# Kernel tuning notes

Measured on AMD Instinct MI355X. Metric: run time of the kernel, lower is better.

Reference implementation:

```python
import jax, jax.numpy as jnp
import numpy as np

N_NODES = 20000
N_EDGES = 160000
B = 200      # num graphs (nodes per graph = 100)
T = 8        # num_tau
A = 10       # action_size
H = 4        # heads
D = 128      # out_channels
R = 4        # num_relations
NCOS = 64


def rgat(x, edge_index, edge_type, W, q, k, b):
    # W: [R, in, H*D]; q, k: [H*D, H]; b: [D]
    xw = jnp.einsum('ni,rio->nro', x, W)              # [N, R, H*D]
    src, dst = edge_index[0], edge_index[1]
    xj = xw[src, edge_type]                            # [E, H*D] gather by edge + relation
    xi = xw[dst, edge_type]                            # [E, H*D]
    alpha = jax.nn.leaky_relu(xi @ q + xj @ k, 0.2)    # [E, H]
    amax = jax.ops.segment_max(alpha, dst, num_segments=N_NODES)
    ex = jnp.exp(alpha - amax[dst])                    # segment softmax over dst
    denom = jax.ops.segment_sum(ex, dst, num_segments=N_NODES)
    a = ex / denom[dst]                                # [E, H]
    msg = (a[:, :, None] * xj.reshape(-1, H, D)).reshape(-1, H * D)
    agg = jax.ops.segment_sum(msg, dst, num_segments=N_NODES).reshape(-1, H, D)
    return agg.mean(axis=1) + b                        # concat=False -> mean over heads


def noisy_linear(z, w, bias, sw, sb, ew, eb):
    # torch convention: w [out, in]
    return z @ (w + sw * ew).T + (bias + sb * eb)


def setup_inputs():
    key = jax.random.key(0)
    ks = jax.random.split(key, 48)
    def rn(i, shape, scale=0.05):
        return jax.random.normal(ks[i], shape, dtype=jnp.float32) * scale
    SIG = 0.017
    inp = {
        'x': jax.random.normal(ks[0], (N_NODES, 2), dtype=jnp.float32),
        'edge_index': jax.random.randint(ks[1], (2, N_EDGES), 0, N_NODES, dtype=jnp.int32),
        'edge_type': jax.random.randint(ks[2], (N_EDGES,), 0, R, dtype=jnp.int32),
        'taus': jax.random.uniform(ks[3], (B, T, 1), dtype=jnp.float32),
        'W1': rn(4, (R, 2, H * D), 0.3), 'q1': rn(5, (H * D, H), 0.05), 'k1': rn(6, (H * D, H), 0.05), 'b1': rn(7, (D,)),
        'W2': rn(8, (R, D, H * D), 0.06), 'q2': rn(9, (H * D, H), 0.05), 'k2': rn(10, (H * D, H), 0.05), 'b2': rn(11, (D,)),
        'cos_w': rn(12, (D, NCOS), 0.1), 'cos_b': rn(13, (D,)),
        'ff1_w': rn(14, (D, D), 0.1), 'ff1_b': rn(15, (D,)),
        'ff1_sw': jnp.full((D, D), SIG, jnp.float32), 'ff1_sb': jnp.full((D,), SIG, jnp.float32),
        'ff1_ew': rn(16, (D, D), 1.0), 'ff1_eb': rn(17, (D,), 1.0),
        'ff2_w': rn(18, (D, D), 0.1), 'ff2_b': rn(19, (D,)),
        'ff2_sw': jnp.full((D, D), SIG, jnp.float32), 'ff2_sb': jnp.full((D,), SIG, jnp.float32),
        'ff2_ew': rn(20, (D, D), 1.0), 'ff2_eb': rn(21, (D,), 1.0),
        'adv_w': rn(22, (A, D), 0.1), 'adv_b': rn(23, (A,)),
        'adv_sw': jnp.full((A, D), SIG, jnp.float32), 'adv_sb': jnp.full((A,), SIG, jnp.float32),
        'adv_ew': rn(24, (A, D), 1.0), 'adv_eb': rn(25, (A,), 1.0),
        'val_w': rn(26, (1, D), 0.1), 'val_b': rn(27, (1,)),
        'val_sw': jnp.full((1, D), SIG, jnp.float32), 'val_sb': jnp.full((1,), SIG, jnp.float32),
        'val_ew': rn(28, (1, D), 1.0), 'val_eb': rn(29, (1,), 1.0),
    }
    return inp


def reference(x, edge_index, edge_type, taus,
              W1, q1, k1, b1, W2, q2, k2, b2, cos_w, cos_b,
              ff1_w, ff1_b, ff1_sw, ff1_sb, ff1_ew, ff1_eb,
              ff2_w, ff2_b, ff2_sw, ff2_sb, ff2_ew, ff2_eb,
              adv_w, adv_b, adv_sw, adv_sb, adv_ew, adv_eb,
              val_w, val_b, val_sw, val_sb, val_ew, val_eb):
    h = jax.nn.selu(rgat(x, edge_index, edge_type, W1, q1, k1, b1))
    h = jax.nn.selu(rgat(h, edge_index, edge_type, W2, q2, k2, b2))
    g = h.reshape(B, N_NODES // B, D).sum(axis=1)      # global_add_pool (block batch_idx)
    pis = jnp.pi * jnp.arange(1, NCOS + 1, dtype=jnp.float32)  # [NCOS]
    cos = jnp.cos(taus * pis)                           # [B, T, NCOS]
    cos_x = jax.nn.relu(cos @ cos_w.T + cos_b)          # [B, T, D]
    z = (g[:, None, :] * cos_x).reshape(B * T, D)
    z = jax.nn.selu(noisy_linear(z, ff1_w, ff1_b, ff1_sw, ff1_sb, ff1_ew, ff1_eb))
    z = jax.nn.selu(noisy_linear(z, ff2_w, ff2_b, ff2_sw, ff2_sb, ff2_ew, ff2_eb))
    adv = noisy_linear(z, adv_w, adv_b, adv_sw, adv_sb, adv_ew, adv_eb)   # [B*T, A]
    val = noisy_linear(z, val_w, val_b, val_sw, val_sb, val_ew, val_eb)   # [B*T, 1]
    out = val + adv - adv.mean(axis=1, keepdims=True)
    return out.reshape(B, T, A), taus
```

## Files before the change

### kernel.cpp

```cpp
#include <hip/hip_runtime.h>
#include <hip/hip_bf16.h>

constexpr long NN = 20000;
constexpr long NE = 160000;
constexpr long BB = 200;
constexpr long TT = 8;
constexpr long GN = 100;

constexpr long O_FLAG = 0;
constexpr long O_X    = 16;                 constexpr long N_X   = 40000;
constexpr long O_TAU  = O_X + N_X;          constexpr long N_TAU = 1600;
constexpr long O_W1   = O_TAU + N_TAU;      constexpr long N_W1  = 4096;
constexpr long O_Q1   = O_W1 + N_W1;        constexpr long N_Q   = 2048;
constexpr long O_K1   = O_Q1 + N_Q;
constexpr long O_B1   = O_K1 + N_Q;         constexpr long N_B   = 128;
constexpr long O_W2   = O_B1 + N_B;         constexpr long N_W2  = 262144;
constexpr long O_Q2   = O_W2 + N_W2;
constexpr long O_K2   = O_Q2 + N_Q;
constexpr long O_B2   = O_K2 + N_Q;
constexpr long O_CW   = O_B2 + N_B;         constexpr long N_CW  = 8192;
constexpr long O_CB   = O_CW + N_CW;
constexpr long O_F1W  = O_CB + N_B;         constexpr long N_FW  = 16384;
constexpr long O_F1B  = O_F1W + N_FW;
constexpr long O_F1SW = O_F1B + N_B;
constexpr long O_F1SB = O_F1SW + N_FW;
constexpr long O_F1EW = O_F1SB + N_B;
constexpr long O_F1EB = O_F1EW + N_FW;
constexpr long O_F2W  = O_F1EB + N_B;
constexpr long O_F2B  = O_F2W + N_FW;
constexpr long O_F2SW = O_F2B + N_B;
constexpr long O_F2SB = O_F2SW + N_FW;
constexpr long O_F2EW = O_F2SB + N_B;
constexpr long O_F2EB = O_F2EW + N_FW;
constexpr long O_AW   = O_F2EB + N_B;       constexpr long N_AW  = 1280;
constexpr long O_AB   = O_AW + N_AW;        constexpr long N_AB  = 16;
constexpr long O_ASW  = O_AB + N_AB;
constexpr long O_ASB  = O_ASW + N_AW;
constexpr long O_AEW  = O_ASB + N_AB;
constexpr long O_AEB  = O_AEW + N_AW;
constexpr long O_VW   = O_AEB + N_AB;       constexpr long N_VW  = 128;
constexpr long O_VB   = O_VW + N_VW;        constexpr long N_VB  = 16;
constexpr long O_VSW  = O_VB + N_VB;
constexpr long O_VSB  = O_VSW + N_VW;
constexpr long O_VEW  = O_VSB + N_VB;
constexpr long O_VEB  = O_VEW + N_VW;
constexpr long O_WQ1  = O_VEB + N_VB;
constexpr long O_WK1  = O_WQ1 + 32;
constexpr long O_WQ2  = O_WK1 + 32;
constexpr long O_WK2  = O_WQ2 + 2048;
constexpr long O_CF1W = O_WK2 + 2048;
constexpr long O_CF1B = O_CF1W + N_FW;
constexpr long O_CF2W = O_CF1B + N_B;
constexpr long O_CF2B = O_CF2W + N_FW;
constexpr long O_CAW  = O_CF2B + N_B;
constexpr long O_CAB  = O_CAW + N_AW;
constexpr long O_CVW  = O_CAB + N_AB;
constexpr long O_CVB  = O_CVW + N_VW;
constexpr long O_AL1  = O_CVB + N_VB;
constexpr long O_AL2  = O_AL1 + NE*4;
constexpr long O_H1   = O_AL2 + NE*4;
constexpr long O_H2   = O_H1 + NN*128;
constexpr long O_G    = O_H2 + NN*128;
constexpr long O_Z0   = O_G + BB*128;
constexpr long O_Z1   = O_Z0 + BB*TT*128;
constexpr long O_Z2   = O_Z1 + BB*TT*128;
constexpr long O_AGG1 = O_Z2 + BB*TT*128;
constexpr long O_DEG  = O_AGG1;
constexpr long O_CUR  = O_DEG + NN;
constexpr long O_ROWP = O_CUR + NN;
constexpr long O_PERM = O_ROWP + NN + 8;
constexpr long O_AGG2 = O_AGG1 + NN*128;
constexpr long O_DEN1 = O_AGG2 + NN*128;
constexpr long O_DEN2 = O_DEN1 + NN*4;
constexpr long O_AMAX1= O_DEN2 + NN*4;
constexpr long O_AMAX2= O_AMAX1 + NN*4;
constexpr long O_XW2  = O_AMAX2 + NN*4;
constexpr long O_END_TABLE = O_XW2 + (NN*4*512)/2;
constexpr long MPAD   = 20096;
constexpr long O_H1B  = O_END_TABLE;
constexpr long O_W2BT = O_H1B + (MPAD*128)/2;
constexpr long O_END2 = O_W2BT + (2048L*128)/2;
constexpr long O_AQ   = O_END2;
constexpr long O_AK   = O_AQ + NN*16;
constexpr long O_END3 = O_AK + NN*16;

constexpr int EMAX = 128;

#define DEVFN __device__ __forceinline__

typedef __attribute__((ext_vector_type(8))) short bf16x8;
typedef __attribute__((ext_vector_type(4))) float f32x4;
typedef __attribute__((ext_vector_type(4))) unsigned short u16x4;

DEVFN float selu_f(float x){ return 1.0507009873554805f * (x > 0.f ? x : 1.6732632423543772f * expm1f(x)); }
DEVFN float lrelu_f(float x){ return x >= 0.f ? x : 0.2f * x; }
DEVFN float bf2f(unsigned short u){ return __uint_as_float(((unsigned)u) << 16); }

__global__ void k_detect(const unsigned short* taus_u16, int* flag){
    if (threadIdx.x == 0){
        int bf = 1;
        for (int i = 0; i < 128; i++){
            if (taus_u16[i] > 0x3F80u){ bf = 0; break; }
        }
        *flag = bf;
    }
}

struct ConvArgs { const void* src[38]; long off[38]; int n[38]; };

__global__ void k_convert(ConvArgs a, float* ws){
    int arr = blockIdx.y;
    long off = a.off[arr];
    if (off < 0) return;
    const void* s = a.src[arr];
    int n = a.n[arr];
    int bf = ((const int*)ws)[0];
    for (int i = blockIdx.x*blockDim.x + threadIdx.x; i < n; i += gridDim.x*blockDim.x){
        float v;
        if (bf){ unsigned short u = ((const unsigned short*)s)[i]; v = bf2f(u); }
        else   { v = ((const float*)s)[i]; }
        ws[off + i] = v;
    }
}

__global__ void k_hist(const int* ei, float* ws){
    long e = (long)blockIdx.x*blockDim.x + threadIdx.x;
    if (e >= NE) return;
    atomicAdd((int*)(ws + O_DEG) + ei[NE + e], 1);
}

__global__ void k_scan(float* ws){
    const int* deg = (const int*)(ws + O_DEG);
    int* rowp = (int*)(ws + O_ROWP);
    __shared__ int part[256];
    int tid = threadIdx.x;
    int base = tid * 79;
    int n = 0; if (base < NN) n = min(79, (int)NN - base);
    int s = 0;
    for (int i = 0; i < n; i++) s += deg[base + i];
    part[tid] = s;
    __syncthreads();
    if (tid == 0){
        int acc = 0;
        for (int i = 0; i < 256; i++){ int t = part[i]; part[i] = acc; acc += t; }
    }
    __syncthreads();
    int acc = part[tid];
    for (int i = 0; i < n; i++){ rowp[base + i] = acc; acc += deg[base + i]; }
    if (tid == 0) rowp[NN] = (int)NE;
}

__global__ void k_scatter(const int* ei, float* ws){
    long e = (long)blockIdx.x*blockDim.x + threadIdx.x;
    if (e >= NE) return;
    int dst = ei[NE + e];
    int pos = atomicAdd((int*)(ws + O_CUR) + dst, 1);
    ((int*)(ws + O_PERM))[((const int*)(ws + O_ROWP))[dst] + pos] = (int)e;
}

__global__ void k_prep(float* ws){
    int phase = blockIdx.y;
    int idx = blockIdx.x*blockDim.x + threadIdx.x;
    if (phase == 0){
        if (idx >= 4160) return;
        long wsrc, qsrc, dst; int ri, h;
        if (idx < 64){
            int t = idx & 31; h = t & 3; ri = t >> 2;
            wsrc = O_W1 + (long)ri*512;
            qsrc = (idx < 32) ? O_Q1 : O_K1;
            dst  = ((idx < 32) ? O_WQ1 : O_WK1) + t;
        } else {
            int t = (idx - 64) & 2047; h = t & 3; ri = t >> 2;
            wsrc = O_W2 + (long)ri*512;
            qsrc = (idx < 2112) ? O_Q2 : O_K2;
            dst  = ((idx < 2112) ? O_WQ2 : O_WK2) + t;
        }
        const float* W = ws + wsrc;
        const float* Q = ws + qsrc;
        float s = 0.f;
        for (int o = 0; o < 512; o++) s += W[o] * Q[o*4 + h];
        ws[dst] = s;
    } else if (phase == 1){
        const long tw[8] = {O_F1W,O_F2W,O_AW,O_VW, O_F1B,O_F2B,O_AB,O_VB};
        const long ts[8] = {O_F1SW,O_F2SW,O_ASW,O_VSW, O_F1SB,O_F2SB,O_ASB,O_VSB};
        const long te[8] = {O_F1EW,O_F2EW,O_AEW,O_VEW, O_F1EB,O_F2EB,O_AEB,O_VEB};
        const long td[8] = {O_CF1W,O_CF2W,O_CAW,O_CVW, O_CF1B,O_CF2B,O_CAB,O_CVB};
        const int  tn[8] = {16384,16384,1280,128, 128,128,10,1};
        const int  tb[8] = {0,16384,32768,34048, 34176,34304,34432,34442};
        int total = 34443;
        for (int i = idx; i < total; i += gridDim.x*blockDim.x){
            int t = 0;
            #pragma unroll
            for (int q = 1; q < 8; q++) if (i >= tb[q]) t = q;
            int j = i - tb[t];
            if (j < tn[t]) ws[td[t] + j] = ws[tw[t] + j] + ws[ts[t] + j]*ws[te[t] + j];
        }
    } else if (phase == 2){
        if (idx >= 262144) return;
        int np = idx & 2047, k = idx >> 11;
        int r = np >> 9, q = np & 511, d = q >> 2, h = q & 3;
        float v = ws[O_W2 + (long)r*65536 + (long)k*512 + h*128 + d];
        ((__hip_bfloat16*)(ws + O_W2BT))[(long)np*128 + k] = __float2bfloat16(v);
    } else {
        if (idx < 6144) ws[O_H1B + (20000L*128)/2 + idx] = 0.f;
    }
}

__global__ void k_node1(const int* ei, const int* et, float* ws){
    __shared__ float wqk[64];
    __shared__ float alc[EMAX][4];
    __shared__ float xsc[EMAX][2];
    __shared__ int   rtc[EMAX];
    __shared__ float sacc[4][4][2];
    __shared__ float den[4], amax[4];
    __shared__ float mred[2][4];
    int n = blockIdx.x, tid = threadIdx.x;
    const int* rowp = (const int*)(ws + O_ROWP);
    const int* perm = (const int*)(ws + O_PERM);
    int e0 = rowp[n], deg = rowp[n+1] - e0;
    if (tid < 64) wqk[tid] = ws[O_WQ1 + tid];
    if (tid < 32) ((float*)sacc)[tid] = 0.f;
    if (tid < 4) den[tid] = 0.f;
    float xd0 = ws[O_X + (long)n*2], xd1 = ws[O_X + (long)n*2 + 1];
    __syncthreads();
    float mx[4] = {-3.0e38f,-3.0e38f,-3.0e38f,-3.0e38f};
    for (int j0 = 0; j0 < deg; j0 += 128){
        int j = j0 + tid;
        if (j < deg){
            int e = perm[e0 + j];
            int src = ei[e], rt = et[e];
            float xs0 = ws[O_X + (long)src*2], xs1 = ws[O_X + (long)src*2 + 1];
            const float* Wq = wqk + rt*8;
            const float* Wk = wqk + 32 + rt*8;
            #pragma unroll
            for (int h = 0; h < 4; h++){
                float a = lrelu_f(xd0*Wq[h] + xd1*Wq[4+h] + xs0*Wk[h] + xs1*Wk[4+h]);
                if (j < EMAX) alc[j][h] = a;
                mx[h] = fmaxf(mx[h], a);
            }
            if (j < EMAX){ xsc[j][0] = xs0; xsc[j][1] = xs1; rtc[j] = rt; }
        }
    }
    #pragma unroll
    for (int off = 32; off > 0; off >>= 1)
        #pragma unroll
        for (int h = 0; h < 4; h++) mx[h] = fmaxf(mx[h], __shfl_xor(mx[h], off));
    if ((tid & 63) == 0)
        #pragma unroll
        for (int h = 0; h < 4; h++) mred[tid >> 6][h] = mx[h];
    __syncthreads();
    if (tid < 4) amax[tid] = fmaxf(mred[0][tid], mred[1][tid]);
    __syncthreads();
    for (int j0 = 0; j0 < deg; j0 += 128){
        int j = j0 + tid;
        if (j < deg){
            float al[4], xs0, xs1; int rt;
            if (j < EMAX){
                #pragma unroll
                for (int h = 0; h < 4; h++) al[h] = alc[j][h];
                xs0 = xsc[j][0]; xs1 = xsc[j][1]; rt = rtc[j];
            } else {
                int e = perm[e0 + j];
                int src = ei[e]; rt = et[e];
                xs0 = ws[O_X + (long)src*2]; xs1 = ws[O_X + (long)src*2 + 1];
                const float* Wq = wqk + rt*8;
                const float* Wk = wqk + 32 + rt*8;
                #pragma unroll
                for (int h = 0; h < 4; h++)
                    al[h] = lrelu_f(xd0*Wq[h] + xd1*Wq[4+h] + xs0*Wk[h] + xs1*Wk[4+h]);
            }
            #pragma unroll
            for (int h = 0; h < 4; h++){
                float ex = expf(al[h] - amax[h]);
                atomicAdd(&den[h], ex);
                atomicAdd(&sacc[rt][h][0], ex*xs0);
                atomicAdd(&sacc[rt][h][1], ex*xs1);
            }
        }
    }
    __syncthreads();
    int d = tid;
    float rden[4];
    #pragma unroll
    for (int h = 0; h < 4; h++) rden[h] = den[h] > 0.f ? 0.25f/den[h] : 0.f;
    float v = 0.f;
    #pragma unroll
    for (int r = 0; r < 4; r++)
        #pragma unroll
        for (int h = 0; h < 4; h++){
            float w0 = ws[O_W1 + r*1024 +        h*128 + d];
            float w1 = ws[O_W1 + r*1024 + 512  + h*128 + d];
            v += rden[h]*(w0*sacc[r][h][0] + w1*sacc[r][h][1]);
        }
    float out = selu_f(v + ws[O_B1 + d]);
    ws[O_H1 + (long)n*128 + d] = out;
    ((__hip_bfloat16*)(ws + O_H1B))[(long)n*128 + d] = __float2bfloat16(out);
}

__global__ void k_aqk(float* ws){
    __shared__ float wq[128*16];
    __shared__ float wk[128*16];
    __shared__ float hl[16][129];
    int tid = threadIdx.x;
    long nb = (long)blockIdx.x * 16;
    #pragma unroll
    for (int c = 0; c < 8; c++){
        int idx = tid + c*256;
        int i = idx >> 4, o = idx & 15;
        int r = o >> 2, h = o & 3;
        wq[i*16 + o] = ws[O_WQ2 + r*512 + i*4 + h];
        wk[i*16 + o] = ws[O_WK2 + r*512 + i*4 + h];
        hl[idx >> 7][idx & 127] = ws[O_H1 + nb*128 + idx];
    }
    __syncthreads();
    int j = tid >> 4, o = tid & 15;
    float aq = 0.f, ak = 0.f;
    #pragma unroll 4
    for (int i = 0; i < 128; i++){
        float hv = hl[j][i];
        aq += hv * wq[i*16 + o];
        ak += hv * wk[i*16 + o];
    }
    ws[O_AQ + (nb + j)*16 + o] = aq;
    ws[O_AK + (nb + j)*16 + o] = ak;
}

__global__ void k_xw2_mfma(float* ws){
    __shared__ __align__(16) unsigned short Ash[128*128];
    __shared__ __align__(16) unsigned short Bsh[128*128];
    const unsigned short* h1b  = (const unsigned short*)(ws + O_H1B);
    const unsigned short* w2bt = (const unsigned short*)(ws + O_W2BT);
    long bm = (long)blockIdx.x * 128;
    long bn = (long)blockIdx.y * 128;
    int tid = threadIdx.x;
    char* Ac = (char*)Ash; char* Bc = (char*)Bsh;
    #pragma unroll
    for (int i = 0; i < 8; i++){
        int c = tid + i*256;
        int row = c >> 4, kb = (c & 15) * 16;
        int off = row*256 + (kb ^ ((row & 7) << 4));
        *(bf16x8*)(Ac + off) = *(const bf16x8*)&h1b [(bm + row)*128 + (c & 15)*8];
        *(bf16x8*)(Bc + off) = *(const bf16x8*)&w2bt[(bn + row)*128 + (c & 15)*8];
    }
    __syncthreads();
    int w = tid >> 6, lane = tid & 63;
    int wm = (w >> 1) * 64, wn = (w & 1) * 64;
    int r16 = lane & 15, kq = lane >> 4;
    f32x4 acc[4][4] = {};
    #pragma unroll
    for (int ks = 0; ks < 4; ks++){
        int kbyte = ks*64 + kq*16;
        bf16x8 a[4], b[4];
        #pragma unroll
        for (int m = 0; m < 4; m++){
            int row = wm + m*16 + r16;
            a[m] = *(const bf16x8*)(Ac + row*256 + (kbyte ^ ((row & 7) << 4)));
        }
        #pragma unroll
        for (int n = 0; n < 4; n++){
            int row = wn + n*16 + r16;
            b[n] = *(const bf16x8*)(Bc + row*256 + (kbyte ^ ((row & 7) << 4)));
        }
        #pragma unroll
        for (int m = 0; m < 4; m++)
            #pragma unroll
            for (int n = 0; n < 4; n++)
                acc[m][n] = __builtin_amdgcn_mfma_f32_16x16x32_bf16(a[m], b[n], acc[m][n], 0, 0, 0);
    }
    __hip_bfloat16* xb = (__hip_bfloat16*)(ws + O_XW2);
    #pragma unroll
    for (int m = 0; m < 4; m++){
        long gr0 = bm + wm + m*16 + kq*4;
        #pragma unroll
        for (int j = 0; j < 4; j++){
            long gr = gr0 + j;
            if (gr < NN){
                #pragma unroll
                for (int n = 0; n < 4; n++){
                    long gc = bn + wn + n*16 + r16;
                    xb[gr*2048 + gc] = __float2bfloat16(acc[m][n][j]);
                }
            }
        }
    }
}

__global__ void k_node2(const int* ei, const int* et, float* ws){
    __shared__ float aq[16];
    __shared__ float exc[EMAX][4];
    __shared__ int   esrt[EMAX];
    __shared__ float den[4], amax[4];
    __shared__ float mred[2][4];
    int n = blockIdx.x, tid = threadIdx.x;
    const int* rowp = (const int*)(ws + O_ROWP);
    const int* perm = (const int*)(ws + O_PERM);
    int e0 = rowp[n], deg = rowp[n+1] - e0;
    if (tid < 16) aq[tid] = ws[O_AQ + (long)n*16 + tid];
    if (tid < 4) den[tid] = 0.f;
    __syncthreads();
    float mx[4] = {-3.0e38f,-3.0e38f,-3.0e38f,-3.0e38f};
    for (int j0 = 0; j0 < deg; j0 += 128){
        int j = j0 + tid;
        if (j < deg){
            int e = perm[e0 + j];
            int src = ei[e], rt = et[e];
            float4 k4 = *(const float4*)&ws[O_AK + (long)src*16 + rt*4];
            float al0 = lrelu_f(aq[rt*4+0] + k4.x);
            float al1 = lrelu_f(aq[rt*4+1] + k4.y);
            float al2 = lrelu_f(aq[rt*4+2] + k4.z);
            float al3 = lrelu_f(aq[rt*4+3] + k4.w);
            if (j < EMAX){
                exc[j][0]=al0; exc[j][1]=al1; exc[j][2]=al2; exc[j][3]=al3;
                esrt[j] = src*4 + rt;
            }
            mx[0]=fmaxf(mx[0],al0); mx[1]=fmaxf(mx[1],al1);
            mx[2]=fmaxf(mx[2],al2); mx[3]=fmaxf(mx[3],al3);
        }
    }
    #pragma unroll
    for (int off = 32; off > 0; off >>= 1)
        #pragma unroll
        for (int h = 0; h < 4; h++) mx[h] = fmaxf(mx[h], __shfl_xor(mx[h], off));
    if ((tid & 63) == 0)
        #pragma unroll
        for (int h = 0; h < 4; h++) mred[tid >> 6][h] = mx[h];
    __syncthreads();
    if (tid < 4) amax[tid] = fmaxf(mred[0][tid], mred[1][tid]);
    __syncthreads();
    for (int j0 = 0; j0 < deg; j0 += 128){
        int j = j0 + tid;
        if (j < deg && j < EMAX){
            #pragma unroll
            for (int h = 0; h < 4; h++){
                float ex = expf(exc[j][h] - amax[h]);
                exc[j][h] = ex;
                atomicAdd(&den[h], ex);
            }
        } else if (j < deg){
            int e = perm[e0 + j];
            int src = ei[e], rt = et[e];
            float4 k4 = *(const float4*)&ws[O_AK + (long)src*16 + rt*4];
            float al[4] = {lrelu_f(aq[rt*4+0]+k4.x), lrelu_f(aq[rt*4+1]+k4.y),
                           lrelu_f(aq[rt*4+2]+k4.z), lrelu_f(aq[rt*4+3]+k4.w)};
            #pragma unroll
            for (int h = 0; h < 4; h++) atomicAdd(&den[h], expf(al[h]-amax[h]));
        }
    }
    __syncthreads();
    int d = tid;
    const unsigned short* xw2 = (const unsigned short*)(ws + O_XW2);
    float acc[4] = {0.f,0.f,0.f,0.f};
    for (int j = 0; j < deg; j++){
        float ex[4]; long sr;
        if (j < EMAX){
            ex[0]=exc[j][0]; ex[1]=exc[j][1]; ex[2]=exc[j][2]; ex[3]=exc[j][3];
            sr = esrt[j];
        } else {
            int e = perm[e0 + j];
            int src = ei[e], rt = et[e];
            float4 k4 = *(const float4*)&ws[O_AK + (long)src*16 + rt*4];
            ex[0]=expf(lrelu_f(aq[rt*4+0]+k4.x)-amax[0]);
            ex[1]=expf(lrelu_f(aq[rt*4+1]+k4.y)-amax[1]);
            ex[2]=expf(lrelu_f(aq[rt*4+2]+k4.z)-amax[2]);
            ex[3]=expf(lrelu_f(aq[rt*4+3]+k4.w)-amax[3]);
            sr = (long)src*4 + rt;
        }
        u16x4 v = *(const u16x4*)(xw2 + sr*512 + (d << 2));
        acc[0] += ex[0]*bf2f(v[0]);
        acc[1] += ex[1]*bf2f(v[1]);
        acc[2] += ex[2]*bf2f(v[2]);
        acc[3] += ex[3]*bf2f(v[3]);
    }
    float v = 0.f;
    #pragma unroll
    for (int h = 0; h < 4; h++){
        float rden = den[h] > 0.f ? 0.25f/den[h] : 0.f;
        v += acc[h]*rden;
    }
    ws[O_H2 + (long)n*128 + d] = selu_f(v + ws[O_B2 + d]);
}

__global__ void k_pool(float* ws){
    int b = blockIdx.x, d = threadIdx.x;
    float s = 0.f;
    for (int j = 0; j < GN; j++) s += ws[O_H2 + ((long)b*GN + j)*128 + d];
    ws[O_G + (long)b*128 + d] = s;
}

__global__ void k_tail(float* ws, void* d_out, const void* taus_raw){
    __shared__ float cs[64];
    __shared__ float row0[128], row1[128], row2[128];
    __shared__ float advs[12];
    int bt = blockIdx.x, t = threadIdx.x;
    int b = bt >> 3;
    if (t < 64){
        float tau = ws[O_TAU + bt];
        cs[t] = cosf(tau * (3.14159265358979323846f * (float)(t + 1)));
    }
    __syncthreads();
    {
        const float* cw = ws + O_CW + (long)t*64;
        float s = ws[O_CB + t];
        for (int c = 0; c < 64; c++) s += cs[c]*cw[c];
        s = fmaxf(s, 0.f);
        row0[t] = ws[O_G + (long)b*128 + t] * s;
    }
    __syncthreads();
    {
        const float* W = ws + O_CF1W + (long)t*128;
        float s = ws[O_CF1B + t];
        for (int i = 0; i < 128; i++) s += row0[i]*W[i];
        row1[t] = selu_f(s);
    }
    __syncthreads();
    {
        const float* W = ws + O_CF2W + (long)t*128;
        float s = ws[O_CF2B + t];
        for (int i = 0; i < 128; i++) s += row1[i]*W[i];
        row2[t] = selu_f(s);
    }
    __syncthreads();
    if (t < 11){
        const float* W = (t < 10) ? (ws + O_CAW + (long)t*128) : (ws + O_CVW);
        float s = (t < 10) ? ws[O_CAB + t] : ws[O_CVB];
        for (int i = 0; i < 128; i++) s += row2[i]*W[i];
        advs[t] = s;
    }
    __syncthreads();
    if (t == 0){
        float m = 0.f;
        #pragma unroll
        for (int a = 0; a < 10; a++) m += advs[a];
        m *= 0.1f;
        float val = advs[10];
        int bf = ((const int*)ws)[0];
        if (bf){
            __hip_bfloat16* out = (__hip_bfloat16*)d_out;
            for (int a = 0; a < 10; a++) out[(long)bt*10 + a] = __float2bfloat16(val + advs[a] - m);
            ((unsigned short*)d_out)[16000 + bt] = ((const unsigned short*)taus_raw)[bt];
        } else {
            float* out = (float*)d_out;
            for (int a = 0; a < 10; a++) out[(long)bt*10 + a] = val + advs[a] - m;
            out[16000 + bt] = ((const float*)taus_raw)[bt];
        }
    }
}

extern "C" void kernel_launch(void* const* d_in, const int* in_sizes, int n_in,
                              void* d_out, int out_size, void* d_ws, size_t ws_size,
                              hipStream_t stream){
    (void)in_sizes; (void)n_in; (void)out_size; (void)ws_size;
    float* ws = (float*)d_ws;
    const int* ei = (const int*)d_in[1];
    const int* et = (const int*)d_in[2];

    hipMemsetAsync(ws + O_DEG, 0, (size_t)(2*NN)*4, stream);

    k_detect<<<1, 64, 0, stream>>>((const unsigned short*)d_in[3], (int*)d_ws);

    k_hist<<<625, 256, 0, stream>>>(ei, ws);
    k_scan<<<1, 256, 0, stream>>>(ws);
    k_scatter<<<625, 256, 0, stream>>>(ei, ws);

    ConvArgs ca;
    static const long conv_o[38] = {
        O_X, -1, -1, O_TAU, O_W1, O_Q1, O_K1, O_B1, O_W2, O_Q2, O_K2, O_B2, O_CW, O_CB,
        O_F1W, O_F1B, O_F1SW, O_F1SB, O_F1EW, O_F1EB,
        O_F2W, O_F2B, O_F2SW, O_F2SB, O_F2EW, O_F2EB,
        O_AW, O_AB, O_ASW, O_ASB, O_AEW, O_AEB,
        O_VW, O_VB, O_VSW, O_VSB, O_VEW, O_VEB };
    static const int conv_n[38] = {
        40000, 0, 0, 1600, 4096, 2048, 2048, 128, 262144, 2048, 2048, 128, 8192, 128,
        16384, 128, 16384, 128, 16384, 128,
        16384, 128, 16384, 128, 16384, 128,
        1280, 10, 1280, 10, 1280, 10,
        128, 1, 128, 1, 128, 1 };
    for (int i = 0; i < 38; i++){ ca.src[i] = d_in[i]; ca.off[i] = conv_o[i]; ca.n[i] = conv_n[i]; }
    k_convert<<<dim3(128, 38), 256, 0, stream>>>(ca, ws);

    k_prep<<<dim3(1024, 4), 256, 0, stream>>>(ws);

    k_node1<<<20000, 128, 0, stream>>>(ei, et, ws);

    k_xw2_mfma<<<dim3(157, 16), 256, 0, stream>>>(ws);
    k_aqk<<<1250, 256, 0, stream>>>(ws);
    k_node2<<<20000, 128, 0, stream>>>(ei, et, ws);

    k_pool<<<200, 128, 0, stream>>>(ws);
    k_tail<<<1600, 128, 0, stream>>>(ws, d_out, d_in[3]);
}
```

Before: 252.9 us.

## Merge small launches, unroll node2 gather, drop fp32 h1 store, fuse pool into tail

```diff
diff --git a/kernel.cpp b/kernel.cpp
--- a/kernel.cpp
+++ b/kernel.cpp
@@ -96,35 +96,16 @@
 DEVFN float lrelu_f(float x){ return x >= 0.f ? x : 0.2f * x; }
 DEVFN float bf2f(unsigned short u){ return __uint_as_float(((unsigned)u) << 16); }
 
-__global__ void k_detect(const unsigned short* taus_u16, int* flag){
-    if (threadIdx.x == 0){
-        int bf = 1;
-        for (int i = 0; i < 128; i++){
-            if (taus_u16[i] > 0x3F80u){ bf = 0; break; }
-        }
-        *flag = bf;
-    }
-}
-
-struct ConvArgs { const void* src[38]; long off[38]; int n[38]; };
-
-__global__ void k_convert(ConvArgs a, float* ws){
-    int arr = blockIdx.y;
-    long off = a.off[arr];
-    if (off < 0) return;
-    const void* s = a.src[arr];
-    int n = a.n[arr];
-    int bf = ((const int*)ws)[0];
-    for (int i = blockIdx.x*blockDim.x + threadIdx.x; i < n; i += gridDim.x*blockDim.x){
-        float v;
-        if (bf){ unsigned short u = ((const unsigned short*)s)[i]; v = bf2f(u); }
-        else   { v = ((const float*)s)[i]; }
-        ws[off + i] = v;
-    }
-}
-
-__global__ void k_hist(const int* ei, float* ws){
-    long e = (long)blockIdx.x*blockDim.x + threadIdx.x;
+__global__ void k_pre(const unsigned short* taus_u16, const int* ei, float* ws){
+    if (blockIdx.x == 0){
+        if (threadIdx.x == 0){
+            int bf = 1;
+            for (int i = 0; i < 128; i++) if (taus_u16[i] > 0x3F80u){ bf = 0; break; }
+            ((int*)ws)[0] = bf;
+        }
+        return;
+    }
+    long e = (long)(blockIdx.x - 1)*blockDim.x + threadIdx.x;
     if (e >= NE) return;
     atomicAdd((int*)(ws + O_DEG) + ei[NE + e], 1);
 }
@@ -150,12 +131,29 @@
     if (tid == 0) rowp[NN] = (int)NE;
 }
 
-__global__ void k_scatter(const int* ei, float* ws){
-    long e = (long)blockIdx.x*blockDim.x + threadIdx.x;
-    if (e >= NE) return;
-    int dst = ei[NE + e];
-    int pos = atomicAdd((int*)(ws + O_CUR) + dst, 1);
-    ((int*)(ws + O_PERM))[((const int*)(ws + O_ROWP))[dst] + pos] = (int)e;
+struct ConvArgs { const void* src[38]; long off[38]; int n[38]; };
+
+__global__ void k_conv_scatter(ConvArgs a, const int* ei, float* ws){
+    int y = blockIdx.y;
+    if (y == 38){
+        long e = (long)blockIdx.x*blockDim.x + threadIdx.x;
+        if (e >= NE) return;
+        int dst = ei[NE + e];
+        int pos = atomicAdd((int*)(ws + O_CUR) + dst, 1);
+        ((int*)(ws + O_PERM))[((const int*)(ws + O_ROWP))[dst] + pos] = (int)e;
+        return;
+    }
+    long off = a.off[y];
+    if (off < 0) return;
+    const void* s = a.src[y];
+    int n = a.n[y];
+    int bf = ((const int*)ws)[0];
+    for (int i = blockIdx.x*blockDim.x + threadIdx.x; i < n; i += gridDim.x*blockDim.x){
+        float v;
+        if (bf){ unsigned short u = ((const unsigned short*)s)[i]; v = bf2f(u); }
+        else   { v = ((const float*)s)[i]; }
+        ws[off + i] = v;
+    }
 }
 
 __global__ void k_prep(float* ws){
@@ -293,7 +291,6 @@
             v += rden[h]*(w0*sacc[r][h][0] + w1*sacc[r][h][1]);
         }
     float out = selu_f(v + ws[O_B1 + d]);
-    ws[O_H1 + (long)n*128 + d] = out;
     ((__hip_bfloat16*)(ws + O_H1B))[(long)n*128 + d] = __float2bfloat16(out);
 }
 
@@ -303,6 +300,7 @@
     __shared__ float hl[16][129];
     int tid = threadIdx.x;
     long nb = (long)blockIdx.x * 16;
+    const unsigned short* h1b = (const unsigned short*)(ws + O_H1B);
     #pragma unroll
     for (int c = 0; c < 8; c++){
         int idx = tid + c*256;
@@ -310,7 +308,7 @@
         int r = o >> 2, h = o & 3;
         wq[i*16 + o] = ws[O_WQ2 + r*512 + i*4 + h];
         wk[i*16 + o] = ws[O_WK2 + r*512 + i*4 + h];
-        hl[idx >> 7][idx & 127] = ws[O_H1 + nb*128 + idx];
+        hl[idx >> 7][idx & 127] = bf2f(h1b[nb*128 + idx]);
     }
     __syncthreads();
     int j = tid >> 4, o = tid & 15;
@@ -449,99 +447,111 @@
     __syncthreads();
     int d = tid;
     const unsigned short* xw2 = (const unsigned short*)(ws + O_XW2);
-    float acc[4] = {0.f,0.f,0.f,0.f};
-    for (int j = 0; j < deg; j++){
-        float ex[4]; long sr;
-        if (j < EMAX){
-            ex[0]=exc[j][0]; ex[1]=exc[j][1]; ex[2]=exc[j][2]; ex[3]=exc[j][3];
-            sr = esrt[j];
-        } else {
-            int e = perm[e0 + j];
-            int src = ei[e], rt = et[e];
-            float4 k4 = *(const float4*)&ws[O_AK + (long)src*16 + rt*4];
-            ex[0]=expf(lrelu_f(aq[rt*4+0]+k4.x)-amax[0]);
-            ex[1]=expf(lrelu_f(aq[rt*4+1]+k4.y)-amax[1]);
-            ex[2]=expf(lrelu_f(aq[rt*4+2]+k4.z)-amax[2]);
-            ex[3]=expf(lrelu_f(aq[rt*4+3]+k4.w)-amax[3]);
-            sr = (long)src*4 + rt;
-        }
+    float a0=0.f, a1=0.f, a2=0.f, a3=0.f;
+    int mdeg = min(deg, EMAX);
+    int j = 0;
+    for (; j + 4 <= mdeg; j += 4){
+        long s0 = esrt[j], s1 = esrt[j+1], s2 = esrt[j+2], s3 = esrt[j+3];
+        u16x4 v0 = *(const u16x4*)(xw2 + s0*512 + (d << 2));
+        u16x4 v1 = *(const u16x4*)(xw2 + s1*512 + (d << 2));
+        u16x4 v2 = *(const u16x4*)(xw2 + s2*512 + (d << 2));
+        u16x4 v3 = *(const u16x4*)(xw2 + s3*512 + (d << 2));
+        a0 += exc[j  ][0]*bf2f(v0[0]); a1 += exc[j  ][1]*bf2f(v0[1]);
+        a2 += exc[j  ][2]*bf2f(v0[2]); a3 += exc[j  ][3]*bf2f(v0[3]);
+        a0 += exc[j+1][0]*bf2f(v1[0]); a1 += exc[j+1][1]*bf2f(v1[1]);
+        a2 += exc[j+1][2]*bf2f(v1[2]); a3 += exc[j+1][3]*bf2f(v1[3]);
+        a0 += exc[j+2][0]*bf2f(v2[0]); a1 += exc[j+2][1]*bf2f(v2[1]);
+        a2 += exc[j+2][2]*bf2f(v2[2]); a3 += exc[j+2][3]*bf2f(v2[3]);
+        a0 += exc[j+3][0]*bf2f(v3[0]); a1 += exc[j+3][1]*bf2f(v3[1]);
+        a2 += exc[j+3][2]*bf2f(v3[2]); a3 += exc[j+3][3]*bf2f(v3[3]);
+    }
+    for (; j < mdeg; j++){
+        long sr = esrt[j];
         u16x4 v = *(const u16x4*)(xw2 + sr*512 + (d << 2));
-        acc[0] += ex[0]*bf2f(v[0]);
-        acc[1] += ex[1]*bf2f(v[1]);
-        acc[2] += ex[2]*bf2f(v[2]);
-        acc[3] += ex[3]*bf2f(v[3]);
-    }
-    float v = 0.f;
-    #pragma unroll
-    for (int h = 0; h < 4; h++){
-        float rden = den[h] > 0.f ? 0.25f/den[h] : 0.f;
-        v += acc[h]*rden;
-    }
+        a0 += exc[j][0]*bf2f(v[0]); a1 += exc[j][1]*bf2f(v[1]);
+        a2 += exc[j][2]*bf2f(v[2]); a3 += exc[j][3]*bf2f(v[3]);
+    }
+    for (j = EMAX; j < deg; j++){
+        int e = perm[e0 + j];
+        int src = ei[e], rt = et[e];
+        float4 k4 = *(const float4*)&ws[O_AK + (long)src*16 + rt*4];
+        float e0h = expf(lrelu_f(aq[rt*4+0]+k4.x)-amax[0]);
+        float e1h = expf(lrelu_f(aq[rt*4+1]+k4.y)-amax[1]);
+        float e2h = expf(lrelu_f(aq[rt*4+2]+k4.z)-amax[2]);
+        float e3h = expf(lrelu_f(aq[rt*4+3]+k4.w)-amax[3]);
+        u16x4 v = *(const u16x4*)(xw2 + ((long)src*4 + rt)*512 + (d << 2));
+        a0 += e0h*bf2f(v[0]); a1 += e1h*bf2f(v[1]);
+        a2 += e2h*bf2f(v[2]); a3 += e3h*bf2f(v[3]);
+    }
+    float rd0 = den[0] > 0.f ? 0.25f/den[0] : 0.f;
+    float rd1 = den[1] > 0.f ? 0.25f/den[1] : 0.f;
+    float rd2 = den[2] > 0.f ? 0.25f/den[2] : 0.f;
+    float rd3 = den[3] > 0.f ? 0.25f/den[3] : 0.f;
+    float v = a0*rd0 + a1*rd1 + a2*rd2 + a3*rd3;
     ws[O_H2 + (long)n*128 + d] = selu_f(v + ws[O_B2 + d]);
 }
 
-__global__ void k_pool(float* ws){
-    int b = blockIdx.x, d = threadIdx.x;
-    float s = 0.f;
-    for (int j = 0; j < GN; j++) s += ws[O_H2 + ((long)b*GN + j)*128 + d];
-    ws[O_G + (long)b*128 + d] = s;
-}
-
 __global__ void k_tail(float* ws, void* d_out, const void* taus_raw){
+    __shared__ float g[128];
     __shared__ float cs[64];
     __shared__ float row0[128], row1[128], row2[128];
     __shared__ float advs[12];
-    int bt = blockIdx.x, t = threadIdx.x;
-    int b = bt >> 3;
-    if (t < 64){
-        float tau = ws[O_TAU + bt];
-        cs[t] = cosf(tau * (3.14159265358979323846f * (float)(t + 1)));
-    }
-    __syncthreads();
-    {
-        const float* cw = ws + O_CW + (long)t*64;
-        float s = ws[O_CB + t];
-        for (int c = 0; c < 64; c++) s += cs[c]*cw[c];
-        s = fmaxf(s, 0.f);
-        row0[t] = ws[O_G + (long)b*128 + t] * s;
-    }
-    __syncthreads();
-    {
-        const float* W = ws + O_CF1W + (long)t*128;
-        float s = ws[O_CF1B + t];
-        for (int i = 0; i < 128; i++) s += row0[i]*W[i];
-        row1[t] = selu_f(s);
-    }
-    __syncthreads();
-    {
-        const float* W = ws + O_CF2W + (long)t*128;
-        float s = ws[O_CF2B + t];
-        for (int i = 0; i < 128; i++) s += row1[i]*W[i];
-        row2[t] = selu_f(s);
-    }
-    __syncthreads();
-    if (t < 11){
-        const float* W = (t < 10) ? (ws + O_CAW + (long)t*128) : (ws + O_CVW);
-        float s = (t < 10) ? ws[O_CAB + t] : ws[O_CVB];
-        for (int i = 0; i < 128; i++) s += row2[i]*W[i];
-        advs[t] = s;
-    }
-    __syncthreads();
-    if (t == 0){
-        float m = 0.f;
-        #pragma unroll
-        for (int a = 0; a < 10; a++) m += advs[a];
-        m *= 0.1f;
-        float val = advs[10];
-        int bf = ((const int*)ws)[0];
-        if (bf){
-            __hip_bfloat16* out = (__hip_bfloat16*)d_out;
-            for (int a = 0; a < 10; a++) out[(long)bt*10 + a] = __float2bfloat16(val + advs[a] - m);
-            ((unsigned short*)d_out)[16000 + bt] = ((const unsigned short*)taus_raw)[bt];
-        } else {
-            float* out = (float*)d_out;
-            for (int a = 0; a < 10; a++) out[(long)bt*10 + a] = val + advs[a] - m;
-            out[16000 + bt] = ((const float*)taus_raw)[bt];
+    int b = blockIdx.x, t = threadIdx.x;
+    float s = 0.f;
+    for (int j = 0; j < GN; j++) s += ws[O_H2 + ((long)b*GN + j)*128 + t];
+    g[t] = s;
+    int bf = ((const int*)ws)[0];
+    for (int tt = 0; tt < TT; tt++){
+        int bt = b*TT + tt;
+        __syncthreads();
+        if (t < 64){
+            float tau = ws[O_TAU + bt];
+            cs[t] = cosf(tau * (3.14159265358979323846f * (float)(t + 1)));
+        }
+        __syncthreads();
+        {
+            const float* cw = ws + O_CW + (long)t*64;
+            float z = ws[O_CB + t];
+            for (int c = 0; c < 64; c++) z += cs[c]*cw[c];
+            row0[t] = g[t] * fmaxf(z, 0.f);
+        }
+        __syncthreads();
+        {
+            const float* W = ws + O_CF1W + (long)t*128;
+            float s1 = ws[O_CF1B + t];
+            for (int i = 0; i < 128; i++) s1 += row0[i]*W[i];
+            row1[t] = selu_f(s1);
+        }
+        __syncthreads();
+        {
+            const float* W = ws + O_CF2W + (long)t*128;
+            float s2 = ws[O_CF2B + t];
+            for (int i = 0; i < 128; i++) s2 += row1[i]*W[i];
+            row2[t] = selu_f(s2);
+        }
+        __syncthreads();
+        if (t < 11){
+            const float* W = (t < 10) ? (ws + O_CAW + (long)t*128) : (ws + O_CVW);
+            float sa = (t < 10) ? ws[O_CAB + t] : ws[O_CVB];
+            for (int i = 0; i < 128; i++) sa += row2[i]*W[i];
+            advs[t] = sa;
+        }
+        __syncthreads();
+        if (t == 0){
+            float m = 0.f;
+            #pragma unroll
+            for (int a = 0; a < 10; a++) m += advs[a];
+            m *= 0.1f;
+            float val = advs[10];
+            if (bf){
+                __hip_bfloat16* out = (__hip_bfloat16*)d_out;
+                for (int a = 0; a < 10; a++) out[(long)bt*10 + a] = __float2bfloat16(val + advs[a] - m);
+                ((unsigned short*)d_out)[16000 + bt] = ((const unsigned short*)taus_raw)[bt];
+            } else {
+                float* out = (float*)d_out;
+                for (int a = 0; a < 10; a++) out[(long)bt*10 + a] = val + advs[a] - m;
+                out[16000 + bt] = ((const float*)taus_raw)[bt];
+            }
         }
     }
 }
@@ -556,11 +566,8 @@
 
     hipMemsetAsync(ws + O_DEG, 0, (size_t)(2*NN)*4, stream);
 
-    k_detect<<<1, 64, 0, stream>>>((const unsigned short*)d_in[3], (int*)d_ws);
-
-    k_hist<<<625, 256, 0, stream>>>(ei, ws);
+    k_pre<<<626, 256, 0, stream>>>((const unsigned short*)d_in[3], ei, ws);
     k_scan<<<1, 256, 0, stream>>>(ws);
-    k_scatter<<<625, 256, 0, stream>>>(ei, ws);
 
     ConvArgs ca;
     static const long conv_o[38] = {
@@ -576,7 +583,7 @@
         1280, 10, 1280, 10, 1280, 10,
         128, 1, 128, 1, 128, 1 };
     for (int i = 0; i < 38; i++){ ca.src[i] = d_in[i]; ca.off[i] = conv_o[i]; ca.n[i] = conv_n[i]; }
-    k_convert<<<dim3(128, 38), 256, 0, stream>>>(ca, ws);
+    k_conv_scatter<<<dim3(625, 39), 256, 0, stream>>>(ca, ei, ws);
 
     k_prep<<<dim3(1024, 4), 256, 0, stream>>>(ws);
 
@@ -586,6 +593,5 @@
     k_aqk<<<1250, 256, 0, stream>>>(ws);
     k_node2<<<20000, 128, 0, stream>>>(ei, et, ws);
 
-    k_pool<<<200, 128, 0, stream>>>(ws);
-    k_tail<<<1600, 128, 0, stream>>>(ws, d_out, d_in[3]);
-}
+    k_tail<<<200, 128, 0, stream>>>(ws, d_out, d_in[3]);
+}
```

New measurement: 263.9 us. 4.3% more time.
